# Kernel tuning notes

Hardware: AMD Instinct MI355X
Metric: run time of the kernel (lower is better)

## Reference

```python
import math
import jax, jax.numpy as jnp
import numpy as np

TAR_MIN, TAR_MAX = 0.0, 1.0
SRC_MIN, SRC_MAX = 0.0, 1.0
NUM_BINS_TAR = 32
NUM_BINS_SRC = 32
SIGMA_TAR = 0.5 * (TAR_MAX - TAR_MIN) / NUM_BINS_TAR
SIGMA_SRC = 0.5 * (SRC_MAX - SRC_MIN) / NUM_BINS_SRC
EPS = 1e-10


def setup_inputs() -> dict:
    key = jax.random.key(0)
    k1, k2 = jax.random.split(key)
    shape = (4, 1, 96, 96, 96)
    tar = jax.random.uniform(k1, shape, dtype=jnp.float32)
    src = jax.random.uniform(k2, shape, dtype=jnp.float32)
    return {"tar": tar, "src": src}


def _minmax_normalise(x, min_out, max_out):
    # per-sample minmax over all non-batch dims; x: (N, P)
    mn = jnp.min(x, axis=1, keepdims=True)
    mx = jnp.max(x, axis=1, keepdims=True)
    return (x - mn) / (mx - mn + 1e-12) * (max_out - min_out) + min_out


def _window(x, bins, sigma):
    # x: (N, P); bins: (B,) -> (N, B, P) Gaussian soft-binning
    d = x[:, None, :] - bins[None, :, None]
    return jnp.exp(-(d * d) / (2.0 * sigma * sigma)) / math.sqrt(2.0 * math.pi) * sigma


def reference(tar, src):
    N = tar.shape[0]
    t = tar[:, 0].reshape(N, -1)  # (N, P)
    s = src[:, 0].reshape(N, -1)
    t = _minmax_normalise(t, TAR_MIN, TAR_MAX)
    s = _minmax_normalise(s, SRC_MIN, SRC_MAX)

    bins_tar = jnp.linspace(TAR_MIN, TAR_MAX, NUM_BINS_TAR, dtype=t.dtype)
    bins_src = jnp.linspace(SRC_MIN, SRC_MAX, NUM_BINS_SRC, dtype=s.dtype)

    wt = _window(t, bins_tar, SIGMA_TAR)  # (N, Bt, P)
    ws = _window(s, bins_src, SIGMA_SRC)  # (N, Bs, P)

    hist_joint = jnp.einsum('bip,bjp->bij', wt, ws)  # (N, Bt, Bs)
    hist_norm = jnp.sum(hist_joint, axis=(1, 2), keepdims=True)
    p_joint = hist_joint / hist_norm

    p_tar = jnp.sum(p_joint, axis=2)  # (N, Bt)
    p_src = jnp.sum(p_joint, axis=1)  # (N, Bs)

    ent_tar = -jnp.sum(p_tar * jnp.log(p_tar + EPS), axis=1)
    ent_src = -jnp.sum(p_src * jnp.log(p_src + EPS), axis=1)
    ent_joint = -jnp.sum(p_joint * jnp.log(p_joint + EPS), axis=(1, 2))

    # normalised=True
    return -jnp.mean((ent_tar + ent_src) / ent_joint)
```

## Files before the change

### kernel.cpp

```cpp
#include <hip/hip_runtime.h>
#include <math.h>

#define N_SAMPLES 4
#define P_ELEMS   (96*96*96)
#define MM_BPS    216
#define MM_T4     1024
#define H_BPS     432
#define H_TILE    2048
#define H_T4      (H_TILE/4)
#define NCOPY     8
#define WS        1.75343855f
#define EPSR      1e-10f

typedef __attribute__((ext_vector_type(8)))  short short8;
typedef __attribute__((ext_vector_type(16))) float float16;

#define PW_COUNT  (N_SAMPLES * H_BPS)


__global__ void __launch_bounds__(256)
k_minmax(const float* __restrict__ tar, const float* __restrict__ src,
         float4* __restrict__ pw, float* __restrict__ histall) {
    __shared__ float4 sred[4];
    int n = blockIdx.y, j = blockIdx.x;
    int t = threadIdx.x;
    const float4* t4 = (const float4*)(tar + (size_t)n * P_ELEMS) + (size_t)j * MM_T4;
    const float4* s4 = (const float4*)(src + (size_t)n * P_ELEMS) + (size_t)j * MM_T4;
    float4 a0 = t4[t], a1 = t4[t + 256], a2 = t4[t + 512], a3 = t4[t + 768];
    float4 b0 = s4[t], b1 = s4[t + 256], b2 = s4[t + 512], b3 = s4[t + 768];
    float mnt = fminf(fminf(fminf(a0.x, a0.y), fminf(a0.z, a0.w)),
                      fminf(fminf(a1.x, a1.y), fminf(a1.z, a1.w)));
    mnt = fminf(mnt, fminf(fminf(fminf(a2.x, a2.y), fminf(a2.z, a2.w)),
                           fminf(fminf(a3.x, a3.y), fminf(a3.z, a3.w))));
    float mxt = fmaxf(fmaxf(fmaxf(a0.x, a0.y), fmaxf(a0.z, a0.w)),
                      fmaxf(fmaxf(a1.x, a1.y), fmaxf(a1.z, a1.w)));
    mxt = fmaxf(mxt, fmaxf(fmaxf(fmaxf(a2.x, a2.y), fmaxf(a2.z, a2.w)),
                           fmaxf(fmaxf(a3.x, a3.y), fmaxf(a3.z, a3.w))));
    float mns = fminf(fminf(fminf(b0.x, b0.y), fminf(b0.z, b0.w)),
                      fminf(fminf(b1.x, b1.y), fminf(b1.z, b1.w)));
    mns = fminf(mns, fminf(fminf(fminf(b2.x, b2.y), fminf(b2.z, b2.w)),
                           fminf(fminf(b3.x, b3.y), fminf(b3.z, b3.w))));
    float mxs = fmaxf(fmaxf(fmaxf(b0.x, b0.y), fmaxf(b0.z, b0.w)),
                      fmaxf(fmaxf(b1.x, b1.y), fmaxf(b1.z, b1.w)));
    mxs = fmaxf(mxs, fmaxf(fmaxf(fmaxf(b2.x, b2.y), fmaxf(b2.z, b2.w)),
                           fmaxf(fmaxf(b3.x, b3.y), fmaxf(b3.z, b3.w))));
    #pragma unroll
    for (int o = 32; o; o >>= 1) {
        mnt = fminf(mnt, __shfl_xor(mnt, o));
        mxt = fmaxf(mxt, __shfl_xor(mxt, o));
        mns = fminf(mns, __shfl_xor(mns, o));
        mxs = fmaxf(mxs, __shfl_xor(mxs, o));
    }
    int lane = t & 63, wave = t >> 6;
    if (lane == 0) sred[wave] = make_float4(mnt, mxt, mns, mxs);
    __syncthreads();
    if (t == 0) {
        float4 v0 = sred[0], v1 = sred[1], v2 = sred[2], v3 = sred[3];
        float4 r;
        r.x = fminf(fminf(v0.x, v1.x), fminf(v2.x, v3.x));
        r.y = fmaxf(fmaxf(v0.y, v1.y), fmaxf(v2.y, v3.y));
        r.z = fminf(fminf(v0.z, v1.z), fminf(v2.z, v3.z));
        r.w = fmaxf(fmaxf(v0.w, v1.w), fmaxf(v2.w, v3.w));
        pw[n * MM_BPS + j] = r;
    }
    int bid = n * MM_BPS + j;
    if (bid < 128) histall[bid * 256 + t] = 0.0f;
}


__global__ void __launch_bounds__(256, 8)
k_hist(const float* __restrict__ tar, const float* __restrict__ src,
       const float4* __restrict__ pw, float* __restrict__ histall) {
    __shared__ __align__(16) float lds[2 * H_TILE];
    __shared__ float4 sred[4];
    __shared__ float bc[4];
    int n = blockIdx.y, j = blockIdx.x;
    int t = threadIdx.x;

    const float4* t4 = (const float4*)(tar + (size_t)n * P_ELEMS) + (size_t)j * H_T4;
    const float4* s4 = (const float4*)(src + (size_t)n * P_ELEMS) + (size_t)j * H_T4;
    float4 a0 = t4[t], a1 = t4[t + 256];
    float4 b0 = s4[t], b1 = s4[t + 256];

    {
        const float4* pwn = pw + n * MM_BPS;
        float mnt = INFINITY, mxt = -INFINITY, mns = INFINITY, mxs = -INFINITY;
        if (t < MM_BPS) {
            float4 v = pwn[t];
            mnt = v.x; mxt = v.y; mns = v.z; mxs = v.w;
        }
        #pragma unroll
        for (int o = 32; o; o >>= 1) {
            mnt = fminf(mnt, __shfl_xor(mnt, o));
            mxt = fmaxf(mxt, __shfl_xor(mxt, o));
            mns = fminf(mns, __shfl_xor(mns, o));
            mxs = fmaxf(mxs, __shfl_xor(mxs, o));
        }
        int lane = t & 63, wave = t >> 6;
        if (lane == 0) sred[wave] = make_float4(mnt, mxt, mns, mxs);
        __syncthreads();
        if (t == 0) {
            float4 v0 = sred[0], v1 = sred[1], v2 = sred[2], v3 = sred[3];
            bc[0] = fminf(fminf(v0.x, v1.x), fminf(v2.x, v3.x));
            bc[1] = fmaxf(fmaxf(v0.y, v1.y), fmaxf(v2.y, v3.y));
            bc[2] = fminf(fminf(v0.z, v1.z), fminf(v2.z, v3.z));
            bc[3] = fmaxf(fmaxf(v0.w, v1.w), fmaxf(v2.w, v3.w));
        }
        __syncthreads();
    }
    float mnt = bc[0], mns = bc[2];
    float fit = 31.0f * WS / (bc[1] - mnt + 1e-12f);
    float fis = 31.0f * WS / (bc[3] - mns + 1e-12f);

    {
        float4 xo, yo;
        xo.x = (a0.x - mnt) * fit; xo.y = (a0.y - mnt) * fit;
        xo.z = (a0.z - mnt) * fit; xo.w = (a0.w - mnt) * fit;
        ((float4*)lds)[t] = xo;
        xo.x = (a1.x - mnt) * fit; xo.y = (a1.y - mnt) * fit;
        xo.z = (a1.z - mnt) * fit; xo.w = (a1.w - mnt) * fit;
        ((float4*)lds)[t + 256] = xo;
        yo.x = (b0.x - mns) * fis; yo.y = (b0.y - mns) * fis;
        yo.z = (b0.z - mns) * fis; yo.w = (b0.w - mns) * fis;
        ((float4*)(lds + H_TILE))[t] = yo;
        yo.x = (b1.x - mns) * fis; yo.y = (b1.y - mns) * fis;
        yo.z = (b1.z - mns) * fis; yo.w = (b1.w - mns) * fis;
        ((float4*)(lds + H_TILE))[t + 256] = yo;
    }
    __syncthreads();

    int lane = t & 63, wave = t >> 6, g = lane >> 5;
    float q = (float)(lane & 31) * WS;
    const float* xb = lds + wave * (H_TILE / 4);
    const float* yb = lds + H_TILE + wave * (H_TILE / 4);

    float16 acc;
    #pragma unroll
    for (int i = 0; i < 16; i++) acc[i] = 0.0f;

    #pragma unroll 4
    for (int it = 0; it < H_TILE / 4 / 16; it++) {
        int kb = it * 16 + g * 8;
        float4 xa = *(const float4*)(xb + kb);
        float4 xc = *(const float4*)(xb + kb + 4);
        float4 ya = *(const float4*)(yb + kb);
        float4 yc = *(const float4*)(yb + kb + 4);
        float xs[8] = {xa.x, xa.y, xa.z, xa.w, xc.x, xc.y, xc.z, xc.w};
        float ys[8] = {ya.x, ya.y, ya.z, ya.w, yc.x, yc.y, yc.z, yc.w};
        unsigned av[8], bv[8];
        #pragma unroll
        for (int jj = 0; jj < 8; jj++) {
            float d = xs[jj] - q;
            float arg = -d * d;
            float w;
            asm("v_exp_f32 %0, %1" : "=v"(w) : "v"(arg));
            av[jj] = __float_as_uint(w);
            d = ys[jj] - q;
            arg = -d * d;
            asm("v_exp_f32 %0, %1" : "=v"(w) : "v"(arg));
            bv[jj] = __float_as_uint(w);
        }
        union { unsigned u[4]; short8 v; } af, bf;
        #pragma unroll
        for (int jj = 0; jj < 4; jj++) {
            af.u[jj] = __builtin_amdgcn_perm(av[2 * jj + 1], av[2 * jj], 0x07060302u);
            bf.u[jj] = __builtin_amdgcn_perm(bv[2 * jj + 1], bv[2 * jj], 0x07060302u);
        }
        acc = __builtin_amdgcn_mfma_f32_32x32x16_bf16(af.v, bf.v, acc, 0, 0, 0);
    }

    __syncthreads();
    {
        float* hw = lds + wave * 1024;
        int col = lane & 31;
        #pragma unroll
        for (int reg = 0; reg < 16; reg++) {
            int row = (reg & 3) + 8 * (reg >> 2) + 4 * g;
            hw[row * 32 + col] = acc[reg];
        }
    }
    __syncthreads();
    float* histn = histall + ((j & (NCOPY - 1)) * N_SAMPLES + n) * 1024;
    for (int bb = t; bb < 1024; bb += 256) {
        float v = lds[bb] + lds[1024 + bb] + lds[2048 + bb] + lds[3072 + bb];
        unsafeAtomicAdd(&histn[bb], v);
    }
}


__global__ void __launch_bounds__(256)
k_final(const float* __restrict__ histall, float* __restrict__ out) {
    __shared__ float sh[4096];
    __shared__ float wres[4];
    int t = threadIdx.x;
    int lane = t & 63, nn = t >> 6;
    float4 h[4];
    float part = 0.0f;
    #pragma unroll
    for (int r = 0; r < 4; r++) {
        float4 s = make_float4(0.f, 0.f, 0.f, 0.f);
        #pragma unroll
        for (int c = 0; c < NCOPY; c++) {
            const float4* h4 = (const float4*)(histall + (c * N_SAMPLES + nn) * 1024);
            float4 v = h4[lane * 4 + r];
            s.x += v.x; s.y += v.y; s.z += v.z; s.w += v.w;
        }
        h[r] = s;
        part += (s.x + s.y) + (s.z + s.w);
    }
    #pragma unroll
    for (int o = 32; o; o >>= 1) part += __shfl_xor(part, o);
    float inv = 1.0f / part;
    float ej = 0.0f;
    #pragma unroll
    for (int r = 0; r < 4; r++) {
        float4 p;
        p.x = h[r].x * inv; p.y = h[r].y * inv; p.z = h[r].z * inv; p.w = h[r].w * inv;
        ((float4*)(sh + nn * 1024))[lane * 4 + r] = p;
        ej -= p.x * __logf(p.x + EPSR) + p.y * __logf(p.y + EPSR)
            + p.z * __logf(p.z + EPSR) + p.w * __logf(p.w + EPSR);
    }
    #pragma unroll
    for (int o = 32; o; o >>= 1) ej += __shfl_xor(ej, o);
    __syncthreads();
    float m = 0.0f;
    if (lane < 32) {
        int row = lane;
        for (int jj = 0; jj < 32; jj++) m += sh[nn * 1024 + row * 32 + ((jj + row) & 31)];
    } else {
        int col = lane - 32;
        for (int i = 0; i < 32; i++) m += sh[nn * 1024 + i * 32 + col];
    }
    float rc = -m * __logf(m + EPSR);
    #pragma unroll
    for (int o = 16; o; o >>= 1) rc += __shfl_xor(rc, o);
    float es = __shfl(rc, 32);
    if (lane == 0) wres[nn] = (rc + es) / ej;
    __syncthreads();
    if (t == 0)
        out[0] = -(wres[0] + wres[1] + wres[2] + wres[3]) * 0.25f;
}

extern "C" void kernel_launch(void* const* d_in, const int* in_sizes, int n_in,
                              void* d_out, int out_size, void* d_ws, size_t ws_size,
                              hipStream_t stream) {
    const float* tar = (const float*)d_in[0];
    const float* src = (const float*)d_in[1];
    float* out = (float*)d_out;
    float4* pw = (float4*)d_ws;
    float* histall = (float*)((char*)d_ws + PW_COUNT * 16);

    k_minmax<<<dim3(MM_BPS, N_SAMPLES), 256, 0, stream>>>(tar, src, pw, histall);
    k_hist<<<dim3(H_BPS, N_SAMPLES), 256, 0, stream>>>(tar, src, pw, histall);
    k_final<<<1, 256, 0, stream>>>(histall, out);
}
```

Baseline: 111.6 us.

## Switch histogram MFMA from 32x32x16 to four 16x16x32 tiles per step

Replaces the single 32x32x16 bf16 MFMA per iteration with a 2x2 grid of 16x16x32 MFMAs. Each lane now handles 16 bins and 8 samples per quad, so each step covers 32 samples instead of 16 and the loop runs half as many iterations. The number of exponentials per sample is unchanged. Occupancy hint lowered from 8 to 6 blocks per CU, and the workspace offset constant is changed. This trades more MFMA issues and register pressure for a different exp/MFMA balance.

Measured after the change: 111.8 us. No clear change (+0.2%).

```diff
diff --git a/kernel.cpp b/kernel.cpp
--- a/kernel.cpp
+++ b/kernel.cpp
@@ -9,13 +9,12 @@
 #define H_TILE    2048
 #define H_T4      (H_TILE/4)
 #define NCOPY     8
+#define PW_SLOTS  1728
 #define WS        1.75343855f
 #define EPSR      1e-10f
 
 typedef __attribute__((ext_vector_type(8)))  short short8;
-typedef __attribute__((ext_vector_type(16))) float float16;
-
-#define PW_COUNT  (N_SAMPLES * H_BPS)
+typedef __attribute__((ext_vector_type(4)))  float floatx4;
 
 
 __global__ void __launch_bounds__(256)
@@ -68,10 +67,25 @@
 }
 
 
-__global__ void __launch_bounds__(256, 8)
+__device__ __forceinline__ void wpack8(const float s[8], float c, unsigned out[4]) {
+    unsigned w[8];
+    #pragma unroll
+    for (int jj = 0; jj < 8; jj++) {
+        float d = s[jj] - c;
+        float arg = -d * d;
+        float e;
+        asm("v_exp_f32 %0, %1" : "=v"(e) : "v"(arg));
+        w[jj] = __float_as_uint(e);
+    }
+    #pragma unroll
+    for (int p = 0; p < 4; p++)
+        out[p] = __builtin_amdgcn_perm(w[2 * p + 1], w[2 * p], 0x07060302u);
+}
+
+__global__ void __launch_bounds__(256, 6)
 k_hist(const float* __restrict__ tar, const float* __restrict__ src,
        const float4* __restrict__ pw, float* __restrict__ histall) {
-    __shared__ __align__(16) float lds[2 * H_TILE];
+    __shared__ __align__(16) float lds[4096];
     __shared__ float4 sred[4];
     __shared__ float bc[4];
     int n = blockIdx.y, j = blockIdx.x;
@@ -129,54 +143,47 @@
     }
     __syncthreads();
 
-    int lane = t & 63, wave = t >> 6, g = lane >> 5;
-    float q = (float)(lane & 31) * WS;
-    const float* xb = lds + wave * (H_TILE / 4);
-    const float* yb = lds + H_TILE + wave * (H_TILE / 4);
-
-    float16 acc;
-    #pragma unroll
-    for (int i = 0; i < 16; i++) acc[i] = 0.0f;
-
-    #pragma unroll 4
-    for (int it = 0; it < H_TILE / 4 / 16; it++) {
-        int kb = it * 16 + g * 8;
+    int lane = t & 63, wave = t >> 6, quad = lane >> 4;
+    float c0 = (float)(lane & 15) * WS;
+    float c1 = c0 + 16.0f * WS;
+    const float* xb = lds + wave * 512;
+    const float* yb = lds + H_TILE + wave * 512;
+
+    floatx4 acc00, acc01, acc10, acc11;
+    #pragma unroll
+    for (int i = 0; i < 4; i++) { acc00[i] = 0.f; acc01[i] = 0.f; acc10[i] = 0.f; acc11[i] = 0.f; }
+
+    #pragma unroll 2
+    for (int it = 0; it < 16; it++) {
+        int kb = it * 32 + quad * 8;
         float4 xa = *(const float4*)(xb + kb);
         float4 xc = *(const float4*)(xb + kb + 4);
         float4 ya = *(const float4*)(yb + kb);
         float4 yc = *(const float4*)(yb + kb + 4);
         float xs[8] = {xa.x, xa.y, xa.z, xa.w, xc.x, xc.y, xc.z, xc.w};
         float ys[8] = {ya.x, ya.y, ya.z, ya.w, yc.x, yc.y, yc.z, yc.w};
-        unsigned av[8], bv[8];
-        #pragma unroll
-        for (int jj = 0; jj < 8; jj++) {
-            float d = xs[jj] - q;
-            float arg = -d * d;
-            float w;
-            asm("v_exp_f32 %0, %1" : "=v"(w) : "v"(arg));
-            av[jj] = __float_as_uint(w);
-            d = ys[jj] - q;
-            arg = -d * d;
-            asm("v_exp_f32 %0, %1" : "=v"(w) : "v"(arg));
-            bv[jj] = __float_as_uint(w);
-        }
-        union { unsigned u[4]; short8 v; } af, bf;
-        #pragma unroll
-        for (int jj = 0; jj < 4; jj++) {
-            af.u[jj] = __builtin_amdgcn_perm(av[2 * jj + 1], av[2 * jj], 0x07060302u);
-            bf.u[jj] = __builtin_amdgcn_perm(bv[2 * jj + 1], bv[2 * jj], 0x07060302u);
-        }
-        acc = __builtin_amdgcn_mfma_f32_32x32x16_bf16(af.v, bf.v, acc, 0, 0, 0);
+        union { unsigned u[4]; short8 v; } A0, A1, B0, B1;
+        wpack8(xs, c0, A0.u);
+        wpack8(xs, c1, A1.u);
+        wpack8(ys, c0, B0.u);
+        wpack8(ys, c1, B1.u);
+        acc00 = __builtin_amdgcn_mfma_f32_16x16x32_bf16(A0.v, B0.v, acc00, 0, 0, 0);
+        acc01 = __builtin_amdgcn_mfma_f32_16x16x32_bf16(A0.v, B1.v, acc01, 0, 0, 0);
+        acc10 = __builtin_amdgcn_mfma_f32_16x16x32_bf16(A1.v, B0.v, acc10, 0, 0, 0);
+        acc11 = __builtin_amdgcn_mfma_f32_16x16x32_bf16(A1.v, B1.v, acc11, 0, 0, 0);
     }
 
     __syncthreads();
     {
         float* hw = lds + wave * 1024;
-        int col = lane & 31;
+        int col = lane & 15;
+        int rbase = quad * 4;
         #pragma unroll
-        for (int reg = 0; reg < 16; reg++) {
-            int row = (reg & 3) + 8 * (reg >> 2) + 4 * g;
-            hw[row * 32 + col] = acc[reg];
+        for (int reg = 0; reg < 4; reg++) {
+            hw[(rbase + reg) * 32 + col]             = acc00[reg];
+            hw[(rbase + reg) * 32 + col + 16]        = acc01[reg];
+            hw[(rbase + reg + 16) * 32 + col]        = acc10[reg];
+            hw[(rbase + reg + 16) * 32 + col + 16]   = acc11[reg];
         }
     }
     __syncthreads();
@@ -248,7 +255,7 @@
     const float* src = (const float*)d_in[1];
     float* out = (float*)d_out;
     float4* pw = (float4*)d_ws;
-    float* histall = (float*)((char*)d_ws + PW_COUNT * 16);
+    float* histall = (float*)((char*)d_ws + PW_SLOTS * 16);
 
     k_minmax<<<dim3(MM_BPS, N_SAMPLES), 256, 0, stream>>>(tar, src, pw, histall);
     k_hist<<<dim3(H_BPS, N_SAMPLES), 256, 0, stream>>>(tar, src, pw, histall);
```
